# Performance work log

Hardware: AMD Instinct MI355X
Metric: run time of the kernel (lower is better)

## Reference

```python
import jax, jax.numpy as jnp
import numpy as np

DIM, NH, HD = 1536, 12, 128
H, W, NFPB = 22, 40, 3
S = H * W * NFPB            # 2640 query tokens
PAST = 12 * H * W           # 10560 cached kv tokens
MAXF = 150                  # rope cache frames
EPS = 1e-6


def rmsnorm(y, g):
    # torch nn.RMSNorm over last dim
    return y * jax.lax.rsqrt(jnp.mean(y * y, axis=-1, keepdims=True) + EPS) * g


def build_rope_cache(freqs):
    # freqs: [MAXF, HD//2] angles -> flat (t,h,w) grid cache [MAXF*H*W, HD]
    hd2 = HD // 2               # 64
    c_h = hd2 // 3              # 21
    c_w = hd2 // 3              # 21
    c_t = hd2 - c_h - c_w       # 22
    f_t = freqs[:MAXF, :c_t]                       # [150, 22]
    f_h = freqs[:H, c_t:c_t + c_h]                 # [22, 21]
    f_w = freqs[:W, c_t + c_h:]                    # [40, 21]
    t_grid = jnp.broadcast_to(f_t[:, None, None, :], (MAXF, H, W, c_t))
    h_grid = jnp.broadcast_to(f_h[None, :, None, :], (MAXF, H, W, c_h))
    w_grid = jnp.broadcast_to(f_w[None, None, :, :], (MAXF, H, W, c_w))
    flat = jnp.concatenate([t_grid, h_grid, w_grid], -1).reshape(-1, hd2)
    return jnp.cos(flat), jnp.sin(flat)            # each [MAXF*H*W, 64]


def apply_rope_interleaved(t, cos, sin):
    # t: [s, n, HD]; cos/sin: [s, HD//2]; is_neox=False -> interleaved pairs
    te = t[..., 0::2]
    to = t[..., 1::2]
    c = cos[:, None, :]
    s = sin[:, None, :]
    oe = te * c - to * s
    oo = to * c + te * s
    return jnp.stack([oe, oo], axis=-1).reshape(t.shape)


def setup_inputs() -> dict:
    key = jax.random.key(0)
    ks = jax.random.split(key, 14)
    sc = 1.0 / np.sqrt(DIM)
    return {
        "x": jax.random.normal(ks[0], (1, S, DIM), jnp.float32),
        "freqs": jax.random.uniform(ks[1], (MAXF, HD // 2), jnp.float32),
        "cached_k": jax.random.normal(ks[2], (PAST, NH, HD), jnp.float32),
        "cached_v": jax.random.normal(ks[3], (PAST, NH, HD), jnp.float32),
        "Wq": jax.random.normal(ks[4], (DIM, DIM), jnp.float32) * sc,
        "bq": jax.random.normal(ks[5], (DIM,), jnp.float32) * 0.01,
        "Wk": jax.random.normal(ks[6], (DIM, DIM), jnp.float32) * sc,
        "bk": jax.random.normal(ks[7], (DIM,), jnp.float32) * 0.01,
        "Wv": jax.random.normal(ks[8], (DIM, DIM), jnp.float32) * sc,
        "bv": jax.random.normal(ks[9], (DIM,), jnp.float32) * 0.01,
        "Wo": jax.random.normal(ks[10], (DIM, DIM), jnp.float32) * sc,
        "bo": jax.random.normal(ks[11], (DIM,), jnp.float32) * 0.01,
        "gq": jnp.ones((DIM,), jnp.float32),
        "gk": jnp.ones((DIM,), jnp.float32),
        "current_start": PAST,
    }


def reference(x, freqs, cached_k, cached_v, Wq, bq, Wk, bk, Wv, bv, Wo, bo, gq, gk, current_start):
    xs = x[0]                                       # [S, DIM], B == 1
    q = rmsnorm(xs @ Wq.T + bq, gq).reshape(S, NH, HD)
    k = rmsnorm(xs @ Wk.T + bk, gk).reshape(S, NH, HD)
    v = (xs @ Wv.T + bv).reshape(S, NH, HD)

    cos_all, sin_all = build_rope_cache(freqs)
    pos = jnp.arange(S, dtype=jnp.int32) + current_start
    cos, sin = cos_all[pos], sin_all[pos]           # [S, 64]
    q = apply_rope_interleaved(q, cos, sin)
    k = apply_rope_interleaved(k, cos, sin)

    k_lin = jnp.concatenate([cached_k, k], axis=0)  # [KV, NH, HD]
    v_lin = jnp.concatenate([cached_v, v], axis=0)

    scale = 1.0 / np.sqrt(HD)
    scores = jnp.einsum("snd,knd->nsk", q, k_lin) * scale   # [NH, S, KV]
    probs = jax.nn.softmax(scores, axis=-1)
    out = jnp.einsum("nsk,knd->snd", probs, v_lin).reshape(S, DIM)
    return (out @ Wo.T + bo)[None]                  # [1, S, DIM]
```

## Files before the change

### kernel.cpp

```cpp
#include <hip/hip_runtime.h>

typedef unsigned short u16;
typedef short short8 __attribute__((ext_vector_type(8)));
typedef short short4b __attribute__((ext_vector_type(4)));
typedef float f32x4 __attribute__((ext_vector_type(4)));
typedef u16 us4 __attribute__((ext_vector_type(4)));
typedef unsigned u32x2 __attribute__((ext_vector_type(2)));

#define DIM   1536
#define NH    12
#define HD    128
#define SQ_   2640
#define SPAD  2688
#define PAST_ 10560
#define LTOT  13200
#define LPAD  13248

__device__ __forceinline__ u16 f2bf(float f){
  unsigned u = __builtin_bit_cast(unsigned, f);
  u += 0x7fffu + ((u >> 16) & 1u);
  return (u16)(u >> 16);
}
__device__ __forceinline__ float bf2f(u16 h){
  unsigned u = ((unsigned)h) << 16;
  return __builtin_bit_cast(float, u);
}
__device__ __forceinline__ unsigned cvtpk_bf16(float lo, float hi){
  unsigned r;
  asm("v_cvt_pk_bf16_f32 %0, %1, %2" : "=v"(r) : "v"(lo), "v"(hi));
  return r;
}
__device__ __forceinline__ void gload_lds16(const void* g, void* l){
  __builtin_amdgcn_global_load_lds(
      (const __attribute__((address_space(1))) void*)g,
      (__attribute__((address_space(3))) void*)l, 16, 0, 0);
}
__device__ __forceinline__ f32x4 mfma16(short4b a, short4b b, f32x4 c){
#if __has_builtin(__builtin_amdgcn_mfma_f32_16x16x16bf16_1k)
  return __builtin_amdgcn_mfma_f32_16x16x16bf16_1k(a, b, c, 0, 0, 0);
#else
  asm("v_mfma_f32_16x16x16_bf16 %0, %1, %2, %0" : "+v"(c) : "v"(a), "v"(b));
  return c;
#endif
}

__global__ void k_cvt(const float* __restrict__ s, u16* __restrict__ d, int n4){
  int i = blockIdx.x * 256 + threadIdx.x;
  if (i < n4){
    float4 f = ((const float4*)s)[i];
    us4 u; u[0]=f2bf(f.x); u[1]=f2bf(f.y); u[2]=f2bf(f.z); u[3]=f2bf(f.w);
    ((us4*)d)[i] = u;
  }
}

__global__ void k_prep_x(const float* __restrict__ x, u16* __restrict__ AB){
  int i = blockIdx.x * 256 + threadIdx.x;
  int e = i * 4;
  us4 u; u[0]=0; u[1]=0; u[2]=0; u[3]=0;
  if (e < SQ_*DIM){
    float4 f = ((const float4*)x)[i];
    u[0]=f2bf(f.x); u[1]=f2bf(f.y); u[2]=f2bf(f.z); u[3]=f2bf(f.w);
  }
  ((us4*)AB)[i] = u;
}

__global__ void k_prep_cache(const float* __restrict__ src, u16* __restrict__ dst, int n4){
  int i = blockIdx.x * 256 + threadIdx.x;
  if (i >= n4) return;
  int e = i * 4;
  if (e < PAST_*DIM){
    float4 f = ((const float4*)src)[i];
    us4 u; u[0]=f2bf(f.x); u[1]=f2bf(f.y); u[2]=f2bf(f.z); u[3]=f2bf(f.w);
    ((us4*)dst)[i] = u;
  } else {
    us4 u; u[0]=0; u[1]=0; u[2]=0; u[3]=0;
    ((us4*)dst)[i - PAST_*DIM/4 + LTOT*DIM/4] = u;
  }
}

__global__ void k_zero(u16* __restrict__ d, int n4){
  int i = blockIdx.x * 256 + threadIdx.x;
  if (i < n4){ us4 u; u[0]=0; u[1]=0; u[2]=0; u[3]=0; ((us4*)d)[i] = u; }
}

__global__ __launch_bounds__(256) void gemm_qkv(
  const u16* __restrict__ A,
  const u16* __restrict__ W0, const u16* __restrict__ W1, const u16* __restrict__ W2,
  const float* __restrict__ b0, const float* __restrict__ b1, const float* __restrict__ b2,
  u16* __restrict__ QL, u16* __restrict__ KL, u16* __restrict__ VA)
{
  __shared__ __align__(16) u16 As[4096];
  __shared__ __align__(16) u16 Bs[4096];
  int mt = blockIdx.x, nt = blockIdx.y;
  int tid = threadIdx.x, lane = tid & 63, w = tid >> 6;
  int wr = w >> 1, wc = w & 1;
  int which = nt / 12;
  const u16*  Bp = which==0 ? W0 : (which==1 ? W1 : W2);
  const float* bp = which==0 ? b0 : (which==1 ? b1 : b2);
  int nloc = (nt % 12) * 128;
  f32x4 acc[4][4];
  #pragma unroll
  for (int i=0;i<4;i++)
    #pragma unroll
    for (int j=0;j<4;j++) acc[i][j] = (f32x4){0.f,0.f,0.f,0.f};

  for (int k0 = 0; k0 < DIM; k0 += 32){
    #pragma unroll
    for (int p=0;p<2;p++){
      int e = (p*256 + tid) * 8;
      int r = e >> 5, c = e & 31;
      gload_lds16(A  + (size_t)(mt*128 + r)*DIM + k0 + c, (char*)As + p*4096 + (w<<10));
      gload_lds16(Bp + (size_t)(nloc   + r)*DIM + k0 + c, (char*)Bs + p*4096 + (w<<10));
    }
    __syncthreads();
    short8 af[4], bfr[4];
    #pragma unroll
    for (int i=0;i<4;i++){
      af[i]  = *(const short8*)&As[(wr*64 + i*16 + (lane&15))*32 + (lane>>4)*8];
      bfr[i] = *(const short8*)&Bs[(wc*64 + i*16 + (lane&15))*32 + (lane>>4)*8];
    }
    #pragma unroll
    for (int i=0;i<4;i++)
      #pragma unroll
      for (int j=0;j<4;j++)
        acc[i][j] = __builtin_amdgcn_mfma_f32_16x16x32_bf16(af[i], bfr[j], acc[i][j], 0,0,0);
    __syncthreads();
  }
  int rbase = mt*128 + wr*64;
  int cbase = nloc + wc*64;
  #pragma unroll
  for (int j=0;j<4;j++){
    int col = cbase + j*16 + (lane&15);
    float bb = bp[col];
    #pragma unroll
    for (int i=0;i<4;i++){
      #pragma unroll
      for (int q=0;q<4;q++){
        int row = rbase + i*16 + (lane>>4)*4 + q;
        if (row < SQ_){
          u16 uv = f2bf(acc[i][j][q] + bb);
          if (which==0)      QL[(size_t)row*DIM + col] = uv;
          else if (which==1) KL[(size_t)row*DIM + col] = uv;
          else               VA[(size_t)(PAST_ + row)*DIM + col] = uv;
        }
      }
    }
  }
}

__global__ __launch_bounds__(256) void gemm_out(
  const u16* __restrict__ A, const u16* __restrict__ W,
  const float* __restrict__ bias, float* __restrict__ out)
{
  __shared__ __align__(16) u16 As[4096];
  __shared__ __align__(16) u16 Bs[4096];
  int mt = blockIdx.x, nt = blockIdx.y;
  int tid = threadIdx.x, lane = tid & 63, w = tid >> 6;
  int wr = w >> 1, wc = w & 1;
  int nloc = nt * 128;
  f32x4 acc[4][4];
  #pragma unroll
  for (int i=0;i<4;i++)
    #pragma unroll
    for (int j=0;j<4;j++) acc[i][j] = (f32x4){0.f,0.f,0.f,0.f};

  for (int k0 = 0; k0 < DIM; k0 += 32){
    #pragma unroll
    for (int p=0;p<2;p++){
      int e = (p*256 + tid) * 8;
      int r = e >> 5, c = e & 31;
      gload_lds16(A + (size_t)(mt*128 + r)*DIM + k0 + c, (char*)As + p*4096 + (w<<10));
      gload_lds16(W + (size_t)(nloc   + r)*DIM + k0 + c, (char*)Bs + p*4096 + (w<<10));
    }
    __syncthreads();
    short8 af[4], bfr[4];
    #pragma unroll
    for (int i=0;i<4;i++){
      af[i]  = *(const short8*)&As[(wr*64 + i*16 + (lane&15))*32 + (lane>>4)*8];
      bfr[i] = *(const short8*)&Bs[(wc*64 + i*16 + (lane&15))*32 + (lane>>4)*8];
    }
    #pragma unroll
    for (int i=0;i<4;i++)
      #pragma unroll
      for (int j=0;j<4;j++)
        acc[i][j] = __builtin_amdgcn_mfma_f32_16x16x32_bf16(af[i], bfr[j], acc[i][j], 0,0,0);
    __syncthreads();
  }
  int rbase = mt*128 + wr*64;
  int cbase = nloc + wc*64;
  #pragma unroll
  for (int j=0;j<4;j++){
    int col = cbase + j*16 + (lane&15);
    float bb = bias[col];
    #pragma unroll
    for (int i=0;i<4;i++){
      #pragma unroll
      for (int q=0;q<4;q++){
        int row = rbase + i*16 + (lane>>4)*4 + q;
        if (row < SQ_) out[(size_t)row*DIM + col] = acc[i][j][q] + bb;
      }
    }
  }
}

__global__ __launch_bounds__(256) void norm_rope(
  const u16* __restrict__ QL, const u16* __restrict__ KL,
  const float* __restrict__ freqs, const float* __restrict__ gq, const float* __restrict__ gk,
  const int* __restrict__ cs,
  u16* __restrict__ Qout, u16* __restrict__ KAout)
{
  int s = blockIdx.x;
  int isk = blockIdx.y;
  int tid = threadIdx.x;
  const u16* src = (isk ? KL : QL) + (size_t)s*DIM + tid*6;
  float y[6];
  #pragma unroll
  for (int t=0;t<6;t++) y[t] = bf2f(src[t]);
  float ss = 0.f;
  #pragma unroll
  for (int t=0;t<6;t++) ss += y[t]*y[t];
  for (int mk=1; mk<64; mk<<=1) ss += __shfl_xor(ss, mk);
  __shared__ float red[4];
  if ((tid & 63) == 0) red[tid>>6] = ss;
  __syncthreads();
  float rn = rsqrtf((red[0]+red[1]+red[2]+red[3]) * (1.0f/1536.0f) + 1e-6f);
  rn *= isk ? 1.0f : 0.12752961954336302f;
  const float* g = (isk ? gk : gq) + tid*6;
  int pos = cs[0] + s;
  int tpos = pos / 880, rem = pos % 880;
  int hh = rem / 40, wp = rem % 40;
  u16 ov[6];
  #pragma unroll
  for (int pi=0; pi<3; pi++){
    int p = tid*3 + pi;
    int i = p & 63;
    int fr = (i < 22) ? tpos : ((i < 43) ? hh : wp);
    float ang = freqs[fr*64 + i];
    float sn, c;
    sincosf(ang, &sn, &c);
    float e  = y[pi*2]   * rn * g[pi*2];
    float od = y[pi*2+1] * rn * g[pi*2+1];
    ov[pi*2]   = f2bf(e*c - od*sn);
    ov[pi*2+1] = f2bf(od*c + e*sn);
  }
  u16* dst = isk ? (KAout + (size_t)(PAST_ + s)*DIM + tid*6)
                 : (Qout  + (size_t)s*DIM + tid*6);
  #pragma unroll
  for (int t=0;t<6;t++) dst[t] = ov[t];
}

__global__ __launch_bounds__(256, 2) void attn(
  const u16* __restrict__ Qf, const u16* __restrict__ KA,
  const u16* __restrict__ VA, u16* __restrict__ OP, float* __restrict__ ML)
{
  __shared__ __align__(16) u16 Ks[2][64*128];
  __shared__ __align__(16) u16 Vt[2][128*64];
  int h = blockIdx.y, qt = blockIdx.x, z = blockIdx.z;
  int tid = threadIdx.x, lane = tid & 63, w = tid >> 6;
  int g = lane >> 4, q = lane & 15;
  int qrow0 = qt*128 + w*32;
  int kvbeg = z ? 6656 : 0;
  int kvend = z ? LPAD : 6656;
  int c0 = (tid >> 4) << 3;
  int r0 = (tid & 15) << 2;

  short8 qa[2][4];
  #pragma unroll
  for (int cq=0;cq<2;cq++){
    const u16* qb = Qf + (size_t)(qrow0 + cq*16 + q)*DIM + h*HD + g*8;
    #pragma unroll
    for (int kt=0;kt<4;kt++) qa[cq][kt] = *(const short8*)(qb + kt*32);
  }
  f32x4 o[2][8];
  #pragma unroll
  for (int cq=0;cq<2;cq++)
    #pragma unroll
    for (int dt=0;dt<8;dt++) o[cq][dt] = (f32x4){0.f,0.f,0.f,0.f};
  float m[2] = {-1e30f,-1e30f};
  float l[2] = {0.f,0.f};

  auto stageK = [&](int kv0, u16* dK){
    #pragma unroll
    for (int p=0;p<4;p++){
      int e = w*2048 + p*512 + lane*8;
      int r = e >> 7;
      int bcol = (e & 127) << 1;
      int sb = bcol ^ ((r & 7) << 4);
      gload_lds16(KA + (size_t)(kv0 + r)*DIM + h*HD + (sb>>1),
                  (char*)dK + w*4096 + p*1024);
    }
  };
  auto loadV = [&](int kv0, short8* vr){
    const u16* vs = VA + (size_t)(kv0 + r0)*DIM + h*HD + c0;
    vr[0] = *(const short8*)(vs);
    vr[1] = *(const short8*)(vs + DIM);
    vr[2] = *(const short8*)(vs + 2*DIM);
    vr[3] = *(const short8*)(vs + 3*DIM);
  };
  auto writeVt = [&](u16* dV, short8* vr){
    #pragma unroll
    for (int j=0;j<8;j++){
      int d = c0 + j;
      int key = ((d & 7) << 4) | (((d >> 3) & 1) << 3);
      int off = d*128 + ((r0*2) ^ key);
      us4 pk; pk[0]=(u16)vr[0][j]; pk[1]=(u16)vr[1][j]; pk[2]=(u16)vr[2][j]; pk[3]=(u16)vr[3][j];
      *(us4*)((char*)dV + off) = pk;
    }
  };

  short8 vr[4];
  int cur = 0;
  stageK(kvbeg, &Ks[0][0]);
  loadV(kvbeg, vr);
  writeVt(&Vt[0][0], vr);
  __syncthreads();

  for (int kv0 = kvbeg; kv0 < kvend; kv0 += 64){
    int nxt = kv0 + 64;
    bool has_next = nxt < kvend;
    if (has_next){
      stageK(nxt, &Ks[cur^1][0]);
      loadV(nxt, vr);
    }
    f32x4 s4[2][4];
    #pragma unroll
    for (int cq=0;cq<2;cq++)
      #pragma unroll
      for (int ct=0;ct<4;ct++) s4[cq][ct] = (f32x4){0.f,0.f,0.f,0.f};
    const u16* ksb = &Ks[cur][0];
    #pragma unroll
    for (int ct=0;ct<4;ct++){
      int row = ct*16 + q;
      int rbyte = row*256, sw = (row & 7) << 4;
      #pragma unroll
      for (int kt=0;kt<4;kt++){
        int b = (kt*64 + (g<<4)) ^ sw;
        short8 kb = *(const short8*)((const char*)ksb + rbyte + b);
        s4[0][ct] = __builtin_amdgcn_mfma_f32_16x16x32_bf16(kb, qa[0][kt], s4[0][ct], 0,0,0);
        s4[1][ct] = __builtin_amdgcn_mfma_f32_16x16x32_bf16(kb, qa[1][kt], s4[1][ct], 0,0,0);
      }
    }
    if (kv0 + 64 > LTOT){
      #pragma unroll
      for (int ct=0;ct<4;ct++)
        #pragma unroll
        for (int j=0;j<4;j++)
          if (kv0 + ct*16 + g*4 + j >= LTOT){ s4[0][ct][j] = -1e30f; s4[1][ct][j] = -1e30f; }
    }
    float rm[2];
    #pragma unroll
    for (int cq=0;cq<2;cq++){
      float a0 = fmaxf(fmaxf(s4[cq][0][0], s4[cq][0][1]), s4[cq][0][2]);
      float a1 = fmaxf(fmaxf(s4[cq][0][3], s4[cq][1][0]), s4[cq][1][1]);
      float a2 = fmaxf(fmaxf(s4[cq][1][2], s4[cq][1][3]), s4[cq][2][0]);
      float a3 = fmaxf(fmaxf(s4[cq][2][1], s4[cq][2][2]), s4[cq][2][3]);
      float a4 = fmaxf(fmaxf(s4[cq][3][0], s4[cq][3][1]), s4[cq][3][2]);
      float r_ = fmaxf(fmaxf(a0, a1), fmaxf(fmaxf(a2, a3), fmaxf(a4, s4[cq][3][3])));
      r_ = fmaxf(r_, __shfl_xor(r_, 16));
      r_ = fmaxf(r_, __shfl_xor(r_, 32));
      rm[cq] = r_;
    }
    if (__any((rm[0] > m[0]+8.f) | (rm[1] > m[1]+8.f))){
      #pragma unroll
      for (int cq=0;cq<2;cq++){
        float mn = fmaxf(m[cq], rm[cq]);
        float al = exp2f(m[cq] - mn);
        m[cq] = mn;
        l[cq] *= al;
        #pragma unroll
        for (int dt=0;dt<8;dt++){
          f32x4 t = o[cq][dt];
          t[0]*=al; t[1]*=al; t[2]*=al; t[3]*=al;
          o[cq][dt] = t;
        }
      }
    }
    short4b pb[2][4];
    #pragma unroll
    for (int cq=0;cq<2;cq++){
      float rs = 0.f;
      #pragma unroll
      for (int ct=0;ct<4;ct++){
        float e0 = exp2f(s4[cq][ct][0] - m[cq]);
        float e1 = exp2f(s4[cq][ct][1] - m[cq]);
        float e2 = exp2f(s4[cq][ct][2] - m[cq]);
        float e3 = exp2f(s4[cq][ct][3] - m[cq]);
        rs += (e0 + e1) + (e2 + e3);
        u32x2 pw = { cvtpk_bf16(e0, e1), cvtpk_bf16(e2, e3) };
        pb[cq][ct] = __builtin_bit_cast(short4b, pw);
      }
      rs += __shfl_xor(rs, 16);
      rs += __shfl_xor(rs, 32);
      l[cq] += rs;
    }
    const u16* vtb = &Vt[cur][0];
    #pragma unroll
    for (int dt=0;dt<8;dt++){
      int d = dt*16 + q;
      int key = ((d & 7) << 4) | (((d >> 3) & 1) << 3);
      int rbyte = d*128;
      #pragma unroll
      for (int ct=0;ct<4;ct++){
        int b = (ct*32 + (g<<3)) ^ key;
        short4b va_ = *(const short4b*)((const char*)vtb + rbyte + b);
        o[0][dt] = mfma16(va_, pb[0][ct], o[0][dt]);
        o[1][dt] = mfma16(va_, pb[1][ct], o[1][dt]);
      }
    }
    if (has_next){
      writeVt(&Vt[cur^1][0], vr);
      __syncthreads();
      cur ^= 1;
    }
  }
  #pragma unroll
  for (int cq=0;cq<2;cq++){
    int row = qrow0 + cq*16 + q;
    size_t ob = ((size_t)(z*SPAD + row)*NH + h)*HD;
    #pragma unroll
    for (int dt=0;dt<8;dt++){
      u32x2 pw = { cvtpk_bf16(o[cq][dt][0], o[cq][dt][1]),
                   cvtpk_bf16(o[cq][dt][2], o[cq][dt][3]) };
      *(u32x2*)&OP[ob + dt*16 + g*4] = pw;
    }
    if (g == 0){
      size_t mb = ((size_t)(z*SPAD + row)*NH + h)*2;
      ML[mb] = m[cq]; ML[mb+1] = l[cq];
    }
  }
}

__global__ void merge_attn(const u16* __restrict__ OP, const float* __restrict__ ML,
                           u16* __restrict__ AB)
{
  int s = blockIdx.x, h = blockIdx.y, d = threadIdx.x;
  size_t i1 = ((size_t)s*NH + h)*2;
  size_t i2 = ((size_t)(SPAD + s)*NH + h)*2;
  float m1 = ML[i1], l1 = ML[i1+1];
  float m2 = ML[i2], l2 = ML[i2+1];
  float M = fmaxf(m1, m2);
  float e1 = exp2f(m1 - M), e2 = exp2f(m2 - M);
  float den = 1.0f / (l1*e1 + l2*e2);
  float o1 = bf2f(OP[((size_t)s*NH + h)*HD + d]);
  float o2 = bf2f(OP[((size_t)(SPAD + s)*NH + h)*HD + d]);
  AB[(size_t)s*DIM + h*HD + d] = f2bf((o1*e1 + o2*e2) * den);
}

extern "C" void kernel_launch(void* const* d_in, const int* in_sizes, int n_in,
                              void* d_out, int out_size, void* d_ws, size_t ws_size,
                              hipStream_t stream) {
  (void)in_sizes; (void)n_in; (void)out_size; (void)ws_size;
  const float* x    = (const float*)d_in[0];
  const float* freqs= (const float*)d_in[1];
  const float* ck   = (const float*)d_in[2];
  const float* cv   = (const float*)d_in[3];
  const float* Wq   = (const float*)d_in[4];
  const float* bq   = (const float*)d_in[5];
  const float* Wk   = (const float*)d_in[6];
  const float* bk   = (const float*)d_in[7];
  const float* Wv   = (const float*)d_in[8];
  const float* bv   = (const float*)d_in[9];
  const float* Wo   = (const float*)d_in[10];
  const float* bo   = (const float*)d_in[11];
  const float* gq   = (const float*)d_in[12];
  const float* gk   = (const float*)d_in[13];
  const int*   cs   = (const int*)d_in[14];
  float* out = (float*)d_out;
  char* ws = (char*)d_ws;

  u16* AB  = (u16*)(ws);
  u16* Wb3 = (u16*)(ws + 8257536);
  u16* QL  = (u16*)(ws + 12976128);
  u16* KA  = (u16*)(ws + 21233664);
  u16* VA  = (u16*)(ws + 61931520);
  u16* Wb0 = (u16*)(ws + 102629376);
  u16* Wb1 = (u16*)(ws + 107347968);
  u16* Wb2 = (u16*)(ws + 112066560);
  u16* KL  = (u16*)(ws + 116785152);
  u16*   OP = (u16*)(ws + 102629376);
  float* ML = (float*)(ws + 119144448);

  k_cvt<<<2304, 256, 0, stream>>>(Wq, Wb0, 589824);
  k_cvt<<<2304, 256, 0, stream>>>(Wk, Wb1, 589824);
  k_cvt<<<2304, 256, 0, stream>>>(Wv, Wb2, 589824);
  k_cvt<<<2304, 256, 0, stream>>>(Wo, Wb3, 589824);
  k_prep_x<<<4032, 256, 0, stream>>>(x, AB);
  k_prep_cache<<<15912, 256, 0, stream>>>(ck, KA, 4073472);
  k_prep_cache<<<15912, 256, 0, stream>>>(cv, VA, 4073472);
  k_zero<<<72, 256, 0, stream>>>(QL + (size_t)SQ_*DIM, 18432);

  gemm_qkv<<<dim3(21,36), 256, 0, stream>>>(AB, Wb0, Wb1, Wb2, bq, bk, bv, QL, KL, VA);
  norm_rope<<<dim3(2640,2), 256, 0, stream>>>(QL, KL, freqs, gq, gk, cs, QL, KA);
  attn<<<dim3(21,12,2), 256, 0, stream>>>(QL, KA, VA, OP, ML);
  merge_attn<<<dim3(2640,12), 128, 0, stream>>>(OP, ML, AB);
  gemm_out<<<dim3(21,12), 256, 0, stream>>>(AB, Wb3, bo, out);
}
```

Measured before the change: 533.4 us.

## Split attention KV into three segments with 32-row tiles and fuse prep launches

Attention now splits the KV range three ways instead of two, giving 756 blocks instead of 504. KV tiles shrink from 64 to 32 rows so LDS per block halves and three blocks can share a CU (launch bounds raised to 3). The z=0 partial output is written straight into AB so the merge kernel reads it in place, and the merge now combines three partials. The weight-conversion and KV-cache-conversion launches are batched into single 2D launches. Smaller tiles mean more barriers and more softmax/rescale overhead per KV element, and the third segment needs more ML storage beyond the old buffer.

```diff
diff --git a/kernel.cpp b/kernel.cpp
--- a/kernel.cpp
+++ b/kernel.cpp
@@ -15,6 +15,8 @@
 #define PAST_ 10560
 #define LTOT  13200
 #define LPAD  13248
+#define KVB   32
+#define KVSEG 4416
 
 __device__ __forceinline__ u16 f2bf(float f){
   unsigned u = __builtin_bit_cast(unsigned, f);
@@ -44,8 +46,14 @@
 #endif
 }
 
-__global__ void k_cvt(const float* __restrict__ s, u16* __restrict__ d, int n4){
+__global__ void k_cvt4(const float* __restrict__ s0, const float* __restrict__ s1,
+                       const float* __restrict__ s2, const float* __restrict__ s3,
+                       u16* __restrict__ d0, u16* __restrict__ d1,
+                       u16* __restrict__ d2, u16* __restrict__ d3, int n4){
   int i = blockIdx.x * 256 + threadIdx.x;
+  int y = blockIdx.y;
+  const float* s = (y==0)?s0:((y==1)?s1:((y==2)?s2:s3));
+  u16* d = (y==0)?d0:((y==1)?d1:((y==2)?d2:d3));
   if (i < n4){
     float4 f = ((const float4*)s)[i];
     us4 u; u[0]=f2bf(f.x); u[1]=f2bf(f.y); u[2]=f2bf(f.z); u[3]=f2bf(f.w);
@@ -64,9 +72,12 @@
   ((us4*)AB)[i] = u;
 }
 
-__global__ void k_prep_cache(const float* __restrict__ src, u16* __restrict__ dst, int n4){
+__global__ void k_prep_kv(const float* __restrict__ ck, const float* __restrict__ cv,
+                          u16* __restrict__ KA, u16* __restrict__ VA, int n4){
   int i = blockIdx.x * 256 + threadIdx.x;
   if (i >= n4) return;
+  const float* src = blockIdx.y ? cv : ck;
+  u16* dst = blockIdx.y ? VA : KA;
   int e = i * 4;
   if (e < PAST_*DIM){
     float4 f = ((const float4*)src)[i];
@@ -249,20 +260,21 @@
   for (int t=0;t<6;t++) dst[t] = ov[t];
 }
 
-__global__ __launch_bounds__(256, 2) void attn(
+__global__ __launch_bounds__(256, 3) void attn(
   const u16* __restrict__ Qf, const u16* __restrict__ KA,
-  const u16* __restrict__ VA, u16* __restrict__ OP, float* __restrict__ ML)
+  const u16* __restrict__ VA, u16* __restrict__ OP0, u16* __restrict__ OP12,
+  float* __restrict__ ML)
 {
-  __shared__ __align__(16) u16 Ks[2][64*128];
-  __shared__ __align__(16) u16 Vt[2][128*64];
+  __shared__ __align__(16) u16 Ks[2][KVB*128];
+  __shared__ __align__(16) u16 Vt[2][128*KVB];
   int h = blockIdx.y, qt = blockIdx.x, z = blockIdx.z;
   int tid = threadIdx.x, lane = tid & 63, w = tid >> 6;
   int g = lane >> 4, q = lane & 15;
   int qrow0 = qt*128 + w*32;
-  int kvbeg = z ? 6656 : 0;
-  int kvend = z ? LPAD : 6656;
-  int c0 = (tid >> 4) << 3;
-  int r0 = (tid & 15) << 2;
+  int kvbeg = z * KVSEG;
+  int kvend = kvbeg + KVSEG;
+  int c0 = (tid >> 3) << 2;
+  int r0 = (tid & 7) << 2;
 
   short8 qa[2][4];
   #pragma unroll
@@ -281,55 +293,55 @@
 
   auto stageK = [&](int kv0, u16* dK){
     #pragma unroll
-    for (int p=0;p<4;p++){
-      int e = w*2048 + p*512 + lane*8;
+    for (int p=0;p<2;p++){
+      int e = w*1024 + p*512 + lane*8;
       int r = e >> 7;
       int bcol = (e & 127) << 1;
       int sb = bcol ^ ((r & 7) << 4);
       gload_lds16(KA + (size_t)(kv0 + r)*DIM + h*HD + (sb>>1),
-                  (char*)dK + w*4096 + p*1024);
+                  (char*)dK + w*2048 + p*1024);
     }
   };
-  auto loadV = [&](int kv0, short8* vr){
+  auto loadV = [&](int kv0, short4b* vr){
     const u16* vs = VA + (size_t)(kv0 + r0)*DIM + h*HD + c0;
-    vr[0] = *(const short8*)(vs);
-    vr[1] = *(const short8*)(vs + DIM);
-    vr[2] = *(const short8*)(vs + 2*DIM);
-    vr[3] = *(const short8*)(vs + 3*DIM);
+    vr[0] = *(const short4b*)(vs);
+    vr[1] = *(const short4b*)(vs + DIM);
+    vr[2] = *(const short4b*)(vs + 2*DIM);
+    vr[3] = *(const short4b*)(vs + 3*DIM);
   };
-  auto writeVt = [&](u16* dV, short8* vr){
-    #pragma unroll
-    for (int j=0;j<8;j++){
+  auto writeVt = [&](u16* dV, short4b* vr){
+    #pragma unroll
+    for (int j=0;j<4;j++){
       int d = c0 + j;
-      int key = ((d & 7) << 4) | (((d >> 3) & 1) << 3);
-      int off = d*128 + ((r0*2) ^ key);
+      int key = ((d & 3) << 4) | (((d >> 2) & 1) << 3);
+      int off = d*64 + ((r0*2) ^ key);
       us4 pk; pk[0]=(u16)vr[0][j]; pk[1]=(u16)vr[1][j]; pk[2]=(u16)vr[2][j]; pk[3]=(u16)vr[3][j];
       *(us4*)((char*)dV + off) = pk;
     }
   };
 
-  short8 vr[4];
+  short4b vr[4];
   int cur = 0;
   stageK(kvbeg, &Ks[0][0]);
   loadV(kvbeg, vr);
   writeVt(&Vt[0][0], vr);
   __syncthreads();
 
-  for (int kv0 = kvbeg; kv0 < kvend; kv0 += 64){
-    int nxt = kv0 + 64;
+  for (int kv0 = kvbeg; kv0 < kvend; kv0 += KVB){
+    int nxt = kv0 + KVB;
     bool has_next = nxt < kvend;
     if (has_next){
       stageK(nxt, &Ks[cur^1][0]);
       loadV(nxt, vr);
     }
-    f32x4 s4[2][4];
+    f32x4 s4[2][2];
     #pragma unroll
     for (int cq=0;cq<2;cq++)
       #pragma unroll
-      for (int ct=0;ct<4;ct++) s4[cq][ct] = (f32x4){0.f,0.f,0.f,0.f};
+      for (int ct=0;ct<2;ct++) s4[cq][ct] = (f32x4){0.f,0.f,0.f,0.f};
     const u16* ksb = &Ks[cur][0];
     #pragma unroll
-    for (int ct=0;ct<4;ct++){
+    for (int ct=0;ct<2;ct++){
       int row = ct*16 + q;
       int rbyte = row*256, sw = (row & 7) << 4;
       #pragma unroll
@@ -340,9 +352,9 @@
         s4[1][ct] = __builtin_amdgcn_mfma_f32_16x16x32_bf16(kb, qa[1][kt], s4[1][ct], 0,0,0);
       }
     }
-    if (kv0 + 64 > LTOT){
-      #pragma unroll
-      for (int ct=0;ct<4;ct++)
+    if (kv0 + KVB > LTOT){
+      #pragma unroll
+      for (int ct=0;ct<2;ct++)
         #pragma unroll
         for (int j=0;j<4;j++)
           if (kv0 + ct*16 + g*4 + j >= LTOT){ s4[0][ct][j] = -1e30f; s4[1][ct][j] = -1e30f; }
@@ -352,10 +364,7 @@
     for (int cq=0;cq<2;cq++){
       float a0 = fmaxf(fmaxf(s4[cq][0][0], s4[cq][0][1]), s4[cq][0][2]);
       float a1 = fmaxf(fmaxf(s4[cq][0][3], s4[cq][1][0]), s4[cq][1][1]);
-      float a2 = fmaxf(fmaxf(s4[cq][1][2], s4[cq][1][3]), s4[cq][2][0]);
-      float a3 = fmaxf(fmaxf(s4[cq][2][1], s4[cq][2][2]), s4[cq][2][3]);
-      float a4 = fmaxf(fmaxf(s4[cq][3][0], s4[cq][3][1]), s4[cq][3][2]);
-      float r_ = fmaxf(fmaxf(a0, a1), fmaxf(fmaxf(a2, a3), fmaxf(a4, s4[cq][3][3])));
+      float r_ = fmaxf(fmaxf(a0, a1), fmaxf(s4[cq][1][2], s4[cq][1][3]));
       r_ = fmaxf(r_, __shfl_xor(r_, 16));
       r_ = fmaxf(r_, __shfl_xor(r_, 32));
       rm[cq] = r_;
@@ -375,12 +384,12 @@
         }
       }
     }
-    short4b pb[2][4];
+    short4b pb[2][2];
     #pragma unroll
     for (int cq=0;cq<2;cq++){
       float rs = 0.f;
       #pragma unroll
-      for (int ct=0;ct<4;ct++){
+      for (int ct=0;ct<2;ct++){
         float e0 = exp2f(s4[cq][ct][0] - m[cq]);
         float e1 = exp2f(s4[cq][ct][1] - m[cq]);
         float e2 = exp2f(s4[cq][ct][2] - m[cq]);
@@ -397,10 +406,10 @@
     #pragma unroll
     for (int dt=0;dt<8;dt++){
       int d = dt*16 + q;
-      int key = ((d & 7) << 4) | (((d >> 3) & 1) << 3);
-      int rbyte = d*128;
-      #pragma unroll
-      for (int ct=0;ct<4;ct++){
+      int key = ((d & 3) << 4) | (((d >> 2) & 1) << 3);
+      int rbyte = d*64;
+      #pragma unroll
+      for (int ct=0;ct<2;ct++){
         int b = (ct*32 + (g<<3)) ^ key;
         short4b va_ = *(const short4b*)((const char*)vtb + rbyte + b);
         o[0][dt] = mfma16(va_, pb[0][ct], o[0][dt]);
@@ -413,15 +422,16 @@
       cur ^= 1;
     }
   }
+  u16* opb = (z == 0) ? OP0 : (OP12 + (size_t)(z-1)*SPAD*NH*HD);
   #pragma unroll
   for (int cq=0;cq<2;cq++){
     int row = qrow0 + cq*16 + q;
-    size_t ob = ((size_t)(z*SPAD + row)*NH + h)*HD;
+    size_t ob = ((size_t)row*NH + h)*HD;
     #pragma unroll
     for (int dt=0;dt<8;dt++){
       u32x2 pw = { cvtpk_bf16(o[cq][dt][0], o[cq][dt][1]),
                    cvtpk_bf16(o[cq][dt][2], o[cq][dt][3]) };
-      *(u32x2*)&OP[ob + dt*16 + g*4] = pw;
+      *(u32x2*)&opb[ob + dt*16 + g*4] = pw;
     }
     if (g == 0){
       size_t mb = ((size_t)(z*SPAD + row)*NH + h)*2;
@@ -430,20 +440,24 @@
   }
 }
 
-__global__ void merge_attn(const u16* __restrict__ OP, const float* __restrict__ ML,
+__global__ void merge_attn(const u16* __restrict__ OP12, const float* __restrict__ ML,
                            u16* __restrict__ AB)
 {
   int s = blockIdx.x, h = blockIdx.y, d = threadIdx.x;
   size_t i1 = ((size_t)s*NH + h)*2;
   size_t i2 = ((size_t)(SPAD + s)*NH + h)*2;
+  size_t i3 = ((size_t)(2*SPAD + s)*NH + h)*2;
   float m1 = ML[i1], l1 = ML[i1+1];
   float m2 = ML[i2], l2 = ML[i2+1];
-  float M = fmaxf(m1, m2);
-  float e1 = exp2f(m1 - M), e2 = exp2f(m2 - M);
-  float den = 1.0f / (l1*e1 + l2*e2);
-  float o1 = bf2f(OP[((size_t)s*NH + h)*HD + d]);
-  float o2 = bf2f(OP[((size_t)(SPAD + s)*NH + h)*HD + d]);
-  AB[(size_t)s*DIM + h*HD + d] = f2bf((o1*e1 + o2*e2) * den);
+  float m3 = ML[i3], l3 = ML[i3+1];
+  float M = fmaxf(fmaxf(m1, m2), m3);
+  float e1 = exp2f(m1 - M), e2 = exp2f(m2 - M), e3 = exp2f(m3 - M);
+  float den = 1.0f / (l1*e1 + l2*e2 + l3*e3);
+  size_t idx = ((size_t)s*NH + h)*HD + d;
+  float o1 = bf2f(AB[idx]);
+  float o2 = bf2f(OP12[idx]);
+  float o3 = bf2f(OP12[(size_t)SPAD*NH*HD + idx]);
+  AB[idx] = f2bf((o1*e1 + o2*e2 + o3*e3) * den);
 }
 
 extern "C" void kernel_launch(void* const* d_in, const int* in_sizes, int n_in,
@@ -477,21 +491,17 @@
   u16* Wb1 = (u16*)(ws + 107347968);
   u16* Wb2 = (u16*)(ws + 112066560);
   u16* KL  = (u16*)(ws + 116785152);
-  u16*   OP = (u16*)(ws + 102629376);
-  float* ML = (float*)(ws + 119144448);
-
-  k_cvt<<<2304, 256, 0, stream>>>(Wq, Wb0, 589824);
-  k_cvt<<<2304, 256, 0, stream>>>(Wk, Wb1, 589824);
-  k_cvt<<<2304, 256, 0, stream>>>(Wv, Wb2, 589824);
-  k_cvt<<<2304, 256, 0, stream>>>(Wo, Wb3, 589824);
+  u16*   OP12 = (u16*)(ws + 102629376);
+  float* ML   = (float*)(ws + 119144448);
+
+  k_cvt4<<<dim3(2304,4), 256, 0, stream>>>(Wq, Wk, Wv, Wo, Wb0, Wb1, Wb2, Wb3, 589824);
   k_prep_x<<<4032, 256, 0, stream>>>(x, AB);
-  k_prep_cache<<<15912, 256, 0, stream>>>(ck, KA, 4073472);
-  k_prep_cache<<<15912, 256, 0, stream>>>(cv, VA, 4073472);
+  k_prep_kv<<<dim3(15912,2), 256, 0, stream>>>(ck, cv, KA, VA, 4073472);
   k_zero<<<72, 256, 0, stream>>>(QL + (size_t)SQ_*DIM, 18432);
 
   gemm_qkv<<<dim3(21,36), 256, 0, stream>>>(AB, Wb0, Wb1, Wb2, bq, bk, bv, QL, KL, VA);
   norm_rope<<<dim3(2640,2), 256, 0, stream>>>(QL, KL, freqs, gq, gk, cs, QL, KA);
-  attn<<<dim3(21,12,2), 256, 0, stream>>>(QL, KA, VA, OP, ML);
-  merge_attn<<<dim3(2640,12), 128, 0, stream>>>(OP, ML, AB);
+  attn<<<dim3(21,12,3), 256, 0, stream>>>(QL, KA, VA, AB, OP12, ML);
+  merge_attn<<<dim3(2640,12), 128, 0, stream>>>(OP12, ML, AB);
   gemm_out<<<dim3(21,12), 256, 0, stream>>>(AB, Wb3, bo, out);
 }
```

New measurement: 544.2 us. 1.02x slower.

## Enlarge attention query tile to 192 rows and split KV into three segments

Applied to the files above, without the earlier changes.

The attention kernel now gives each wave 48 query rows (three 16-row groups) instead of 32, so every K/V tile staged in LDS feeds more MFMAs. The KV range is split into three equal segments of 4416, with the grid changed to 14x12x3. The merge step is extended to three partials, and the z=0 partial is written straight into the AB buffer so it can be merged in place. It also raises wave priority around the MFMA loops and fuses the weight and KV-cache conversion launches into single multi-plane kernels. The cost is more accumulator registers under launch_bounds(256,2), which risks spills or lower occupancy, and a lot of padded query rows (14*192 = 2688).

```diff
diff --git a/kernel.cpp b/kernel.cpp
--- a/kernel.cpp
+++ b/kernel.cpp
@@ -15,6 +15,8 @@
 #define PAST_ 10560
 #define LTOT  13200
 #define LPAD  13248
+#define KVSEG 4416
+#define CQ    3
 
 __device__ __forceinline__ u16 f2bf(float f){
   unsigned u = __builtin_bit_cast(unsigned, f);
@@ -44,8 +46,14 @@
 #endif
 }
 
-__global__ void k_cvt(const float* __restrict__ s, u16* __restrict__ d, int n4){
+__global__ void k_cvt4(const float* __restrict__ s0, const float* __restrict__ s1,
+                       const float* __restrict__ s2, const float* __restrict__ s3,
+                       u16* __restrict__ d0, u16* __restrict__ d1,
+                       u16* __restrict__ d2, u16* __restrict__ d3, int n4){
   int i = blockIdx.x * 256 + threadIdx.x;
+  int y = blockIdx.y;
+  const float* s = (y==0)?s0:((y==1)?s1:((y==2)?s2:s3));
+  u16* d = (y==0)?d0:((y==1)?d1:((y==2)?d2:d3));
   if (i < n4){
     float4 f = ((const float4*)s)[i];
     us4 u; u[0]=f2bf(f.x); u[1]=f2bf(f.y); u[2]=f2bf(f.z); u[3]=f2bf(f.w);
@@ -64,9 +72,12 @@
   ((us4*)AB)[i] = u;
 }
 
-__global__ void k_prep_cache(const float* __restrict__ src, u16* __restrict__ dst, int n4){
+__global__ void k_prep_kv(const float* __restrict__ ck, const float* __restrict__ cv,
+                          u16* __restrict__ KA, u16* __restrict__ VA, int n4){
   int i = blockIdx.x * 256 + threadIdx.x;
   if (i >= n4) return;
+  const float* src = blockIdx.y ? cv : ck;
+  u16* dst = blockIdx.y ? VA : KA;
   int e = i * 4;
   if (e < PAST_*DIM){
     float4 f = ((const float4*)src)[i];
@@ -251,33 +262,34 @@
 
 __global__ __launch_bounds__(256, 2) void attn(
   const u16* __restrict__ Qf, const u16* __restrict__ KA,
-  const u16* __restrict__ VA, u16* __restrict__ OP, float* __restrict__ ML)
+  const u16* __restrict__ VA, u16* __restrict__ OP0, u16* __restrict__ OP12,
+  float* __restrict__ ML)
 {
   __shared__ __align__(16) u16 Ks[2][64*128];
   __shared__ __align__(16) u16 Vt[2][128*64];
   int h = blockIdx.y, qt = blockIdx.x, z = blockIdx.z;
   int tid = threadIdx.x, lane = tid & 63, w = tid >> 6;
   int g = lane >> 4, q = lane & 15;
-  int qrow0 = qt*128 + w*32;
-  int kvbeg = z ? 6656 : 0;
-  int kvend = z ? LPAD : 6656;
+  int qrow0 = qt*192 + w*48;
+  int kvbeg = z * KVSEG;
+  int kvend = kvbeg + KVSEG;
   int c0 = (tid >> 4) << 3;
   int r0 = (tid & 15) << 2;
 
-  short8 qa[2][4];
-  #pragma unroll
-  for (int cq=0;cq<2;cq++){
+  short8 qa[CQ][4];
+  #pragma unroll
+  for (int cq=0;cq<CQ;cq++){
     const u16* qb = Qf + (size_t)(qrow0 + cq*16 + q)*DIM + h*HD + g*8;
     #pragma unroll
     for (int kt=0;kt<4;kt++) qa[cq][kt] = *(const short8*)(qb + kt*32);
   }
-  f32x4 o[2][8];
-  #pragma unroll
-  for (int cq=0;cq<2;cq++)
+  f32x4 o[CQ][8];
+  #pragma unroll
+  for (int cq=0;cq<CQ;cq++)
     #pragma unroll
     for (int dt=0;dt<8;dt++) o[cq][dt] = (f32x4){0.f,0.f,0.f,0.f};
-  float m[2] = {-1e30f,-1e30f};
-  float l[2] = {0.f,0.f};
+  float m[CQ] = {-1e30f,-1e30f,-1e30f};
+  float l[CQ] = {0.f,0.f,0.f};
 
   auto stageK = [&](int kv0, u16* dK){
     #pragma unroll
@@ -322,12 +334,13 @@
       stageK(nxt, &Ks[cur^1][0]);
       loadV(nxt, vr);
     }
-    f32x4 s4[2][4];
-    #pragma unroll
-    for (int cq=0;cq<2;cq++)
+    f32x4 s4[CQ][4];
+    #pragma unroll
+    for (int cq=0;cq<CQ;cq++)
       #pragma unroll
       for (int ct=0;ct<4;ct++) s4[cq][ct] = (f32x4){0.f,0.f,0.f,0.f};
     const u16* ksb = &Ks[cur][0];
+    __builtin_amdgcn_s_setprio(1);
     #pragma unroll
     for (int ct=0;ct<4;ct++){
       int row = ct*16 + q;
@@ -336,20 +349,25 @@
       for (int kt=0;kt<4;kt++){
         int b = (kt*64 + (g<<4)) ^ sw;
         short8 kb = *(const short8*)((const char*)ksb + rbyte + b);
-        s4[0][ct] = __builtin_amdgcn_mfma_f32_16x16x32_bf16(kb, qa[0][kt], s4[0][ct], 0,0,0);
-        s4[1][ct] = __builtin_amdgcn_mfma_f32_16x16x32_bf16(kb, qa[1][kt], s4[1][ct], 0,0,0);
+        #pragma unroll
+        for (int cq=0;cq<CQ;cq++)
+          s4[cq][ct] = __builtin_amdgcn_mfma_f32_16x16x32_bf16(kb, qa[cq][kt], s4[cq][ct], 0,0,0);
       }
     }
+    __builtin_amdgcn_s_setprio(0);
     if (kv0 + 64 > LTOT){
       #pragma unroll
       for (int ct=0;ct<4;ct++)
         #pragma unroll
         for (int j=0;j<4;j++)
-          if (kv0 + ct*16 + g*4 + j >= LTOT){ s4[0][ct][j] = -1e30f; s4[1][ct][j] = -1e30f; }
-    }
-    float rm[2];
-    #pragma unroll
-    for (int cq=0;cq<2;cq++){
+          if (kv0 + ct*16 + g*4 + j >= LTOT){
+            #pragma unroll
+            for (int cq=0;cq<CQ;cq++) s4[cq][ct][j] = -1e30f;
+          }
+    }
+    float rm[CQ];
+    #pragma unroll
+    for (int cq=0;cq<CQ;cq++){
       float a0 = fmaxf(fmaxf(s4[cq][0][0], s4[cq][0][1]), s4[cq][0][2]);
       float a1 = fmaxf(fmaxf(s4[cq][0][3], s4[cq][1][0]), s4[cq][1][1]);
       float a2 = fmaxf(fmaxf(s4[cq][1][2], s4[cq][1][3]), s4[cq][2][0]);
@@ -360,9 +378,12 @@
       r_ = fmaxf(r_, __shfl_xor(r_, 32));
       rm[cq] = r_;
     }
-    if (__any((rm[0] > m[0]+8.f) | (rm[1] > m[1]+8.f))){
-      #pragma unroll
-      for (int cq=0;cq<2;cq++){
+    bool need = false;
+    #pragma unroll
+    for (int cq=0;cq<CQ;cq++) need |= (rm[cq] > m[cq]+8.f);
+    if (__any(need)){
+      #pragma unroll
+      for (int cq=0;cq<CQ;cq++){
         float mn = fmaxf(m[cq], rm[cq]);
         float al = exp2f(m[cq] - mn);
         m[cq] = mn;
@@ -375,9 +396,9 @@
         }
       }
     }
-    short4b pb[2][4];
-    #pragma unroll
-    for (int cq=0;cq<2;cq++){
+    short4b pb[CQ][4];
+    #pragma unroll
+    for (int cq=0;cq<CQ;cq++){
       float rs = 0.f;
       #pragma unroll
       for (int ct=0;ct<4;ct++){
@@ -394,6 +415,7 @@
       l[cq] += rs;
     }
     const u16* vtb = &Vt[cur][0];
+    __builtin_amdgcn_s_setprio(1);
     #pragma unroll
     for (int dt=0;dt<8;dt++){
       int d = dt*16 + q;
@@ -403,25 +425,28 @@
       for (int ct=0;ct<4;ct++){
         int b = (ct*32 + (g<<3)) ^ key;
         short4b va_ = *(const short4b*)((const char*)vtb + rbyte + b);
-        o[0][dt] = mfma16(va_, pb[0][ct], o[0][dt]);
-        o[1][dt] = mfma16(va_, pb[1][ct], o[1][dt]);
+        #pragma unroll
+        for (int cq=0;cq<CQ;cq++)
+          o[cq][dt] = mfma16(va_, pb[cq][ct], o[cq][dt]);
       }
     }
+    __builtin_amdgcn_s_setprio(0);
     if (has_next){
       writeVt(&Vt[cur^1][0], vr);
       __syncthreads();
       cur ^= 1;
     }
   }
-  #pragma unroll
-  for (int cq=0;cq<2;cq++){
+  u16* opb = (z == 0) ? OP0 : (OP12 + (size_t)(z-1)*SPAD*NH*HD);
+  #pragma unroll
+  for (int cq=0;cq<CQ;cq++){
     int row = qrow0 + cq*16 + q;
-    size_t ob = ((size_t)(z*SPAD + row)*NH + h)*HD;
+    size_t ob = ((size_t)row*NH + h)*HD;
     #pragma unroll
     for (int dt=0;dt<8;dt++){
       u32x2 pw = { cvtpk_bf16(o[cq][dt][0], o[cq][dt][1]),
                    cvtpk_bf16(o[cq][dt][2], o[cq][dt][3]) };
-      *(u32x2*)&OP[ob + dt*16 + g*4] = pw;
+      *(u32x2*)&opb[ob + dt*16 + g*4] = pw;
     }
     if (g == 0){
       size_t mb = ((size_t)(z*SPAD + row)*NH + h)*2;
@@ -430,20 +455,24 @@
   }
 }
 
-__global__ void merge_attn(const u16* __restrict__ OP, const float* __restrict__ ML,
+__global__ void merge_attn(const u16* __restrict__ OP12, const float* __restrict__ ML,
                            u16* __restrict__ AB)
 {
   int s = blockIdx.x, h = blockIdx.y, d = threadIdx.x;
   size_t i1 = ((size_t)s*NH + h)*2;
   size_t i2 = ((size_t)(SPAD + s)*NH + h)*2;
+  size_t i3 = ((size_t)(2*SPAD + s)*NH + h)*2;
   float m1 = ML[i1], l1 = ML[i1+1];
   float m2 = ML[i2], l2 = ML[i2+1];
-  float M = fmaxf(m1, m2);
-  float e1 = exp2f(m1 - M), e2 = exp2f(m2 - M);
-  float den = 1.0f / (l1*e1 + l2*e2);
-  float o1 = bf2f(OP[((size_t)s*NH + h)*HD + d]);
-  float o2 = bf2f(OP[((size_t)(SPAD + s)*NH + h)*HD + d]);
-  AB[(size_t)s*DIM + h*HD + d] = f2bf((o1*e1 + o2*e2) * den);
+  float m3 = ML[i3], l3 = ML[i3+1];
+  float M = fmaxf(fmaxf(m1, m2), m3);
+  float e1 = exp2f(m1 - M), e2 = exp2f(m2 - M), e3 = exp2f(m3 - M);
+  float den = 1.0f / (l1*e1 + l2*e2 + l3*e3);
+  size_t idx = ((size_t)s*NH + h)*HD + d;
+  float o1 = bf2f(AB[idx]);
+  float o2 = bf2f(OP12[idx]);
+  float o3 = bf2f(OP12[(size_t)SPAD*NH*HD + idx]);
+  AB[idx] = f2bf((o1*e1 + o2*e2 + o3*e3) * den);
 }
 
 extern "C" void kernel_launch(void* const* d_in, const int* in_sizes, int n_in,
@@ -477,21 +506,17 @@
   u16* Wb1 = (u16*)(ws + 107347968);
   u16* Wb2 = (u16*)(ws + 112066560);
   u16* KL  = (u16*)(ws + 116785152);
-  u16*   OP = (u16*)(ws + 102629376);
-  float* ML = (float*)(ws + 119144448);
-
-  k_cvt<<<2304, 256, 0, stream>>>(Wq, Wb0, 589824);
-  k_cvt<<<2304, 256, 0, stream>>>(Wk, Wb1, 589824);
-  k_cvt<<<2304, 256, 0, stream>>>(Wv, Wb2, 589824);
-  k_cvt<<<2304, 256, 0, stream>>>(Wo, Wb3, 589824);
+  u16*   OP12 = (u16*)(ws + 102629376);
+  float* ML   = (float*)(ws + 119144448);
+
+  k_cvt4<<<dim3(2304,4), 256, 0, stream>>>(Wq, Wk, Wv, Wo, Wb0, Wb1, Wb2, Wb3, 589824);
   k_prep_x<<<4032, 256, 0, stream>>>(x, AB);
-  k_prep_cache<<<15912, 256, 0, stream>>>(ck, KA, 4073472);
-  k_prep_cache<<<15912, 256, 0, stream>>>(cv, VA, 4073472);
+  k_prep_kv<<<dim3(15912,2), 256, 0, stream>>>(ck, cv, KA, VA, 4073472);
   k_zero<<<72, 256, 0, stream>>>(QL + (size_t)SQ_*DIM, 18432);
 
   gemm_qkv<<<dim3(21,36), 256, 0, stream>>>(AB, Wb0, Wb1, Wb2, bq, bk, bv, QL, KL, VA);
   norm_rope<<<dim3(2640,2), 256, 0, stream>>>(QL, KL, freqs, gq, gk, cs, QL, KA);
-  attn<<<dim3(21,12,2), 256, 0, stream>>>(QL, KA, VA, OP, ML);
-  merge_attn<<<dim3(2640,12), 128, 0, stream>>>(OP, ML, AB);
+  attn<<<dim3(14,12,3), 256, 0, stream>>>(QL, KA, VA, AB, OP12, ML);
+  merge_attn<<<dim3(2640,12), 128, 0, stream>>>(OP12, ML, AB);
   gemm_out<<<dim3(21,12), 256, 0, stream>>>(AB, Wb3, bo, out);
 }
```

New measurement: 556.2 us. 1.04x slower.
